# Optimization experiments

Hardware: AMD Instinct MI355X
Metric: run time of the kernel (lower is better)

## Reference

```python
import jax, jax.numpy as jnp
import numpy as np

E = 512        # embedding_dim
HEADS = 8
PD = 32        # patch_dim
STRIDE = 16    # unfold stride (hard-coded in source)
P = 16         # max regions per image (padded)
NCLS = 3       # num_classes
LN_EPS = 1e-5


def layer_norm(x, g, b):
    mu = x.mean(-1, keepdims=True)
    v = ((x - mu) ** 2).mean(-1, keepdims=True)
    return (x - mu) / jnp.sqrt(v + LN_EPS) * g + b


def patch2vec(x, Wr, br):
    # x: [N, C, PD, PD]; AdaptiveAvgPool3d to (C//4, PD//2, PD//2) with exact
    # integer ratios == block-mean pooling, then Linear(fvector, E).
    N, C, H, W = x.shape
    y = x.reshape(N, C // 4, 4, H // 2, 2, W // 2, 2).mean(axis=(2, 4, 6))
    return y.reshape(N, -1) @ Wr.T + br


def mha(q_in, kv_in, Wqkv, bqkv, Wo, bo):
    # torch nn.MultiheadAttention, batch_first=True
    B, Pq, _ = q_in.shape
    L = kv_in.shape[1]
    hd = E // HEADS
    Wq, Wk, Wv = Wqkv[:E], Wqkv[E:2 * E], Wqkv[2 * E:]
    bq, bk, bv = bqkv[:E], bqkv[E:2 * E], bqkv[2 * E:]
    q = (q_in @ Wq.T + bq).reshape(B, Pq, HEADS, hd)
    k = (kv_in @ Wk.T + bk).reshape(B, L, HEADS, hd)
    v = (kv_in @ Wv.T + bv).reshape(B, L, HEADS, hd)
    scores = jnp.einsum('bphd,blhd->bhpl', q, k) / jnp.sqrt(jnp.asarray(hd, q.dtype))
    attn = jax.nn.softmax(scores, axis=-1)
    out = jnp.einsum('bhpl,blhd->bphd', attn, v).reshape(B, Pq, E)
    return out @ Wo.T + bo


def setup_inputs() -> dict:
    key = jax.random.key(0)
    ks = jax.random.split(key, 12)
    B, C, H, W = 8, 64, 256, 256
    fv = (C // 4) * (PD // 2) * (PD // 2)  # 4096
    s = lambda n: 1.0 / np.sqrt(n)
    return {
        'features': jax.random.normal(ks[0], (B, C, H, W), jnp.float32),
        'probs': jax.random.uniform(ks[1], (B, NCLS, H, W), jnp.float32),
        'patches': jax.random.normal(ks[2], (B, P, C, PD, PD), jnp.float32),
        'masks': jax.random.randint(ks[3], (B, H, W), 0, P + 1, jnp.int32),
        'ln_g': jnp.ones((E,), jnp.float32),
        'ln_b': jnp.zeros((E,), jnp.float32),
        'Wr': jax.random.normal(ks[4], (E, fv), jnp.float32) * s(fv),
        'br': jnp.zeros((E,), jnp.float32),
        'Wqkv': jax.random.normal(ks[5], (3 * E, E), jnp.float32) * s(E),
        'bqkv': jnp.zeros((3 * E,), jnp.float32),
        'Wo': jax.random.normal(ks[6], (E, E), jnp.float32) * s(E),
        'bo': jnp.zeros((E,), jnp.float32),
        'Wm': jax.random.normal(ks[7], (E, E), jnp.float32) * s(E),
        'bm': jnp.zeros((E,), jnp.float32),
        'Wc': jax.random.normal(ks[8], (NCLS - 1, E), jnp.float32) * s(E),
        'bc': jnp.zeros((NCLS - 1,), jnp.float32),
    }


def reference(features, probs, patches, masks, ln_g, ln_b, Wr, br,
              Wqkv, bqkv, Wo, bo, Wm, bm, Wc, bc):
    B, C, H, W = features.shape
    # ---- unfold features into overlapping PDxPD blocks, stride 16 ----
    n = (H - PD) // STRIDE + 1  # 15
    rows = (jnp.arange(n) * STRIDE)[:, None] + jnp.arange(PD)[None, :]  # [n, PD]
    xb = features[:, :, rows, :]          # [B, C, n, PD, W]
    blocks = xb[:, :, :, :, rows]         # [B, C, n, PD, n, PD]
    blocks = blocks.transpose(0, 2, 4, 1, 3, 5).reshape(B, n * n, C, PD, PD)
    L = n * n

    # ---- shared Patch2vec embedding + shared LayerNorm ----
    pe = layer_norm(patch2vec(patches.reshape(B * P, C, PD, PD), Wr, br).reshape(B, P, E), ln_g, ln_b)
    be = layer_norm(patch2vec(blocks.reshape(B * L, C, PD, PD), Wr, br).reshape(B, L, E), ln_g, ln_b)

    # ---- attention + residual MLP ----
    attn = mha(pe, be, Wqkv, bqkv, Wo, bo)
    res = layer_norm(attn + pe, ln_g, ln_b)
    x = jax.nn.gelu(res @ Wm.T + bm, approximate=False) + res
    outs = x @ Wc.T + bc  # [B, P, 2]

    # ---- vectorized masked reclassify (regions are disjoint) ----
    labels = masks  # [B, H, W], 0 = background, 1..P = regions
    seg = (labels.astype(jnp.int32) + jnp.arange(B, dtype=jnp.int32)[:, None, None] * (P + 1)).reshape(-1)
    pr = probs.transpose(0, 2, 3, 1).reshape(-1, NCLS)
    sums = jax.ops.segment_sum(pr, seg, num_segments=B * (P + 1)).reshape(B, P + 1, NCLS)
    cnt = jax.ops.segment_sum(jnp.ones((pr.shape[0],), pr.dtype), seg, num_segments=B * (P + 1)).reshape(B, P + 1)
    mean = sums / jnp.maximum(cnt, 1.0)[..., None] + 1e-6  # orig_mean_logits per region
    ml = mean[:, 1:, :]  # [B, P, NCLS], region labels 1..P <-> logits 0..P-1
    new0 = ml[..., 0] / (0.5 * (ml[..., 1] + ml[..., 2])) * outs.mean(-1)
    newv = jnp.stack([new0, outs[..., 0], outs[..., 1]], axis=-1)  # [B, P, 3]
    newv_full = jnp.concatenate([jnp.zeros((B, 1, NCLS), newv.dtype), newv], axis=1)
    vals = newv_full[jnp.arange(B)[:, None], labels.reshape(B, -1)]  # [B, H*W, 3]
    vals = vals.reshape(B, H, W, NCLS).transpose(0, 3, 1, 2)
    return jnp.where((labels > 0)[:, None, :, :], vals, probs)
```

## Files before the change

kernel.cpp:

```cpp
#include <hip/hip_runtime.h>
#include <stdint.h>


typedef __attribute__((ext_vector_type(8))) short bf16x8;
typedef __attribute__((ext_vector_type(4))) float f32x4;

__device__ __forceinline__ unsigned short f2bf(float x) {
    union { float f; unsigned u; } v; v.f = x;
    unsigned r = v.u + 0x7FFFu + ((v.u >> 16) & 1u);
    return (unsigned short)(r >> 16);
}
__device__ __forceinline__ float bf2f(unsigned short x) {
    union { unsigned u; float f; } v; v.u = ((unsigned)x) << 16; return v.f;
}

__device__ __forceinline__ void g2l16(const unsigned short* g, unsigned short* l) {
    __builtin_amdgcn_global_load_lds(
        (const __attribute__((address_space(1))) unsigned int*)g,
        (__attribute__((address_space(3))) unsigned int*)l, 16, 0, 0);
}

__global__ __launch_bounds__(256) void k_pool_features(
    const float* __restrict__ f, unsigned short* __restrict__ gp)
{
    unsigned t = blockIdx.x * 256u + threadIdx.x;
    unsigned q = t & 127u, r = (t >> 7) & 127u, g = (t >> 14) & 15u, b = t >> 18;
    const float2* f2 = (const float2*)f;
    float s = 0.f;
    unsigned cb = b * 64u + g * 4u;
#pragma unroll
    for (int j = 0; j < 4; ++j) {
#pragma unroll
        for (int a = 0; a < 2; ++a) {
            unsigned idx = ((cb + j) * 256u + 2u * r + a) * 256u + 2u * q;
            float2 v = f2[idx >> 1];
            s += v.x + v.y;
        }
    }
    gp[t] = f2bf(s * 0.0625f);
}

__global__ __launch_bounds__(256) void k_pool_patches(
    const float* __restrict__ p, unsigned short* __restrict__ Xb)
{
    unsigned t = blockIdx.x * 256u + threadIdx.x;
    unsigned i = t & 4095u, row = t >> 12;
    unsigned q = i & 15u, r = (i >> 4) & 15u, g = i >> 8;
    const float2* p2 = (const float2*)p;
    float s = 0.f;
    unsigned cb = row * 64u + g * 4u;
#pragma unroll
    for (int j = 0; j < 4; ++j) {
#pragma unroll
        for (int a = 0; a < 2; ++a) {
            unsigned idx = ((cb + j) * 32u + 2u * r + a) * 32u + 2u * q;
            float2 v = p2[idx >> 1];
            s += v.x + v.y;
        }
    }
    Xb[(size_t)row * 4096 + i] = f2bf(s * 0.0625f);
}

__global__ __launch_bounds__(256) void k_gather_blocks(
    const unsigned short* __restrict__ Gp, unsigned short* __restrict__ Xb)
{
    unsigned t = blockIdx.x * 256u + threadIdx.x;
    unsigned grp = t & 511u, row_rel = t >> 9;
    unsigned k0 = grp * 8u;
    unsigned g = k0 >> 8, r = (k0 >> 4) & 15u, q0 = k0 & 15u;
    unsigned b = row_rel / 225u;
    unsigned ij = row_rel - b * 225u;
    unsigned i = ij / 15u, j = ij - i * 15u;
    size_t src = ((size_t)(b * 16u + g) * 128u + i * 8u + r) * 128u + j * 8u + q0;
    size_t dst = (size_t)(128u + row_rel) * 4096u + k0;
    *(uint4*)(Xb + dst) = *(const uint4*)(Gp + src);
}

__global__ __launch_bounds__(256) void k_f2bf_all(
    const float* __restrict__ Wr, const float* __restrict__ Wqkv,
    const float* __restrict__ Wo, const float* __restrict__ Wm,
    unsigned short* __restrict__ oWr, unsigned short* __restrict__ oWqkv,
    unsigned short* __restrict__ oWo, unsigned short* __restrict__ oWm)
{
    int t = blockIdx.x * 256 + threadIdx.x;
    const float* src; unsigned short* dst; int i;
    if (t < 524288)      { src = Wr;   dst = oWr;   i = t; }
    else if (t < 720896) { src = Wqkv; dst = oWqkv; i = t - 524288; }
    else if (t < 786432) { src = Wo;   dst = oWo;   i = t - 720896; }
    else                 { src = Wm;   dst = oWm;   i = t - 786432; }
    float4 v = ((const float4*)src)[i];
    ushort4 o;
    o.x = f2bf(v.x); o.y = f2bf(v.y); o.z = f2bf(v.z); o.w = f2bf(v.w);
    ((ushort4*)dst)[i] = o;
}

__global__ __launch_bounds__(256) void k_gemm128(
    const unsigned short* __restrict__ A, const unsigned short* __restrict__ Bw,
    const float* __restrict__ bias, float* __restrict__ C,
    int M, int N, int K, int klen)
{
    __shared__ __align__(16) unsigned short As[128 * 32];
    __shared__ __align__(16) unsigned short Bs[128 * 32];
    const int tid = threadIdx.x, w = tid >> 6, lane = tid & 63;
    const int nt = blockIdx.x, mt = blockIdx.y, ks = blockIdx.z;
    const int kbase = ks * klen;
    const int l15 = lane & 15, kq = (lane >> 4) * 8;
    const int wm = (w >> 1) * 64, wn = (w & 1) * 64;
    const int srow0 = w * 32, lrow = lane >> 2, lcol = (lane & 3) * 8;

    f32x4 acc[4][4];
#pragma unroll
    for (int i = 0; i < 4; ++i)
#pragma unroll
        for (int j = 0; j < 4; ++j) acc[i][j] = (f32x4){0.f, 0.f, 0.f, 0.f};

    int arow0 = mt * 128, brow0 = nt * 128;
    for (int k0 = 0; k0 < klen; k0 += 32) {
        int kk = kbase + k0;
#pragma unroll
        for (int c = 0; c < 2; ++c) {
            int r = srow0 + c * 16 + lrow;
            int ga = arow0 + r; if (ga > M - 1) ga = M - 1;
            g2l16(A + (size_t)ga * K + kk + lcol, &As[(srow0 + c * 16) * 32]);
            g2l16(Bw + (size_t)(brow0 + r) * K + kk + lcol, &Bs[(srow0 + c * 16) * 32]);
        }
        __syncthreads();
        bf16x8 af[4], bf[4];
#pragma unroll
        for (int i = 0; i < 4; ++i) {
            af[i] = *(const bf16x8*)&As[(wm + 16 * i + l15) * 32 + kq];
            bf[i] = *(const bf16x8*)&Bs[(wn + 16 * i + l15) * 32 + kq];
        }
#pragma unroll
        for (int i = 0; i < 4; ++i)
#pragma unroll
            for (int j = 0; j < 4; ++j)
                acc[i][j] = __builtin_amdgcn_mfma_f32_16x16x32_bf16(af[i], bf[j], acc[i][j], 0, 0, 0);
        __syncthreads();
    }
    float* Cp = C + (size_t)ks * M * N;
#pragma unroll
    for (int i = 0; i < 4; ++i) {
        int rowb = mt * 128 + wm + i * 16 + (lane >> 4) * 4;
#pragma unroll
        for (int j = 0; j < 4; ++j) {
            int col = nt * 128 + wn + j * 16 + l15;
            float bv = bias ? bias[col] : 0.f;
#pragma unroll
            for (int r = 0; r < 4; ++r) {
                int row = rowb + r;
                if (row < M) Cp[(size_t)row * N + col] = acc[i][j][r] + bv;
            }
        }
    }
}

__global__ __launch_bounds__(256) void k_gemm_nt(
    const unsigned short* __restrict__ A, const unsigned short* __restrict__ Bw,
    const float* __restrict__ bias, float* __restrict__ C,
    int M, int N, int K)
{
    __shared__ __align__(16) unsigned short As[64 * 32];
    __shared__ __align__(16) unsigned short Bs[64 * 32];
    const int tid = threadIdx.x;
    const int bm = blockIdx.y, bn = blockIdx.x;
    const int wave = tid >> 6, lane = tid & 63;
    const int wm = (wave >> 1) * 32, wn = (wave & 1) * 32;
    const int l15 = lane & 15, kq = (lane >> 4) * 8;
    const int srow = tid >> 2, scol = (tid & 3) * 8;
    const unsigned short* Ap = A + (size_t)(bm * 64 + srow) * K + scol;
    const unsigned short* Bp = Bw + (size_t)(bn * 64 + srow) * K + scol;

    f32x4 acc[2][2];
#pragma unroll
    for (int i = 0; i < 2; ++i)
#pragma unroll
        for (int j = 0; j < 2; ++j) acc[i][j] = (f32x4){0.f, 0.f, 0.f, 0.f};

    for (int k0 = 0; k0 < K; k0 += 32) {
        *(uint4*)&As[srow * 32 + scol] = *(const uint4*)(Ap + k0);
        *(uint4*)&Bs[srow * 32 + scol] = *(const uint4*)(Bp + k0);
        __syncthreads();
        bf16x8 a0 = *(const bf16x8*)&As[(wm + l15) * 32 + kq];
        bf16x8 a1 = *(const bf16x8*)&As[(wm + 16 + l15) * 32 + kq];
        bf16x8 b0 = *(const bf16x8*)&Bs[(wn + l15) * 32 + kq];
        bf16x8 b1 = *(const bf16x8*)&Bs[(wn + 16 + l15) * 32 + kq];
        acc[0][0] = __builtin_amdgcn_mfma_f32_16x16x32_bf16(a0, b0, acc[0][0], 0, 0, 0);
        acc[0][1] = __builtin_amdgcn_mfma_f32_16x16x32_bf16(a0, b1, acc[0][1], 0, 0, 0);
        acc[1][0] = __builtin_amdgcn_mfma_f32_16x16x32_bf16(a1, b0, acc[1][0], 0, 0, 0);
        acc[1][1] = __builtin_amdgcn_mfma_f32_16x16x32_bf16(a1, b1, acc[1][1], 0, 0, 0);
        __syncthreads();
    }
#pragma unroll
    for (int it = 0; it < 2; ++it) {
        int rowb = bm * 64 + wm + it * 16 + (lane >> 4) * 4;
#pragma unroll
        for (int iu = 0; iu < 2; ++iu) {
            int col = bn * 64 + wn + iu * 16 + l15;
            float bv = bias[col];
#pragma unroll
            for (int r = 0; r < 4; ++r) {
                int row = rowb + r;
                if (row < M) C[(size_t)row * N + col] = acc[it][iu][r] + bv;
            }
        }
    }
}

__global__ __launch_bounds__(256) void k_lnred(
    const float* __restrict__ Yp, const float* __restrict__ br,
    const float* __restrict__ gg, const float* __restrict__ bb,
    float* __restrict__ outF, unsigned short* __restrict__ outB, int rows)
{
    int wave = threadIdx.x >> 6, lane = threadIdx.x & 63;
    int row = blockIdx.x * 4 + wave;
    if (row >= rows) return;
    size_t base = (size_t)row * 512 + lane * 8;
    float v[8];
    { const float* bp = br + lane * 8;
      float4 a = *(const float4*)bp, b = *(const float4*)(bp + 4);
      v[0]=a.x; v[1]=a.y; v[2]=a.z; v[3]=a.w; v[4]=b.x; v[5]=b.y; v[6]=b.z; v[7]=b.w; }
#pragma unroll
    for (int s = 0; s < 4; ++s) {
        const float* xp = Yp + (size_t)s * rows * 512 + base;
        float4 a = *(const float4*)xp, b = *(const float4*)(xp + 4);
        v[0]+=a.x; v[1]+=a.y; v[2]+=a.z; v[3]+=a.w; v[4]+=b.x; v[5]+=b.y; v[6]+=b.z; v[7]+=b.w;
    }
    float s = 0.f;
#pragma unroll
    for (int i = 0; i < 8; ++i) s += v[i];
#pragma unroll
    for (int m = 32; m; m >>= 1) s += __shfl_xor(s, m, 64);
    float mu = s * (1.f / 512.f);
    float sq = 0.f;
#pragma unroll
    for (int i = 0; i < 8; ++i) { float d = v[i] - mu; sq += d * d; }
#pragma unroll
    for (int m = 32; m; m >>= 1) sq += __shfl_xor(sq, m, 64);
    float rstd = rsqrtf(sq * (1.f / 512.f) + 1e-5f);
    const float* gp = gg + lane * 8;
    const float* bp2 = bb + lane * 8;
    float4 g0 = *(const float4*)gp, g1 = *(const float4*)(gp + 4);
    float4 b0 = *(const float4*)bp2, b1 = *(const float4*)(bp2 + 4);
    float ga[8] = {g0.x,g0.y,g0.z,g0.w,g1.x,g1.y,g1.z,g1.w};
    float ba[8] = {b0.x,b0.y,b0.z,b0.w,b1.x,b1.y,b1.z,b1.w};
    float o[8];
#pragma unroll
    for (int i = 0; i < 8; ++i) o[i] = (v[i] - mu) * rstd * ga[i] + ba[i];
    float* ofp = outF + base;
    float4 w0; w0.x=o[0]; w0.y=o[1]; w0.z=o[2]; w0.w=o[3];
    float4 w1; w1.x=o[4]; w1.y=o[5]; w1.z=o[6]; w1.w=o[7];
    *(float4*)ofp = w0; *(float4*)(ofp + 4) = w1;
    unsigned short* obp = outB + base;
    ushort4 u0, u1;
    u0.x=f2bf(o[0]); u0.y=f2bf(o[1]); u0.z=f2bf(o[2]); u0.w=f2bf(o[3]);
    u1.x=f2bf(o[4]); u1.y=f2bf(o[5]); u1.z=f2bf(o[6]); u1.w=f2bf(o[7]);
    ((ushort4*)obp)[0] = u0; ((ushort4*)obp)[1] = u1;
}

__global__ __launch_bounds__(256) void k_ln(
    const float* __restrict__ X, const float* __restrict__ R,
    const float* __restrict__ gg, const float* __restrict__ bb,
    float* __restrict__ outF, unsigned short* __restrict__ outB, int rows)
{
    int wave = threadIdx.x >> 6, lane = threadIdx.x & 63;
    int row = blockIdx.x * 4 + wave;
    if (row >= rows) return;
    size_t base = (size_t)row * 512 + lane * 8;
    const float* xp = X + base;
    float v[8];
    { float4 a = *(const float4*)xp, b = *(const float4*)(xp + 4);
      v[0]=a.x; v[1]=a.y; v[2]=a.z; v[3]=a.w; v[4]=b.x; v[5]=b.y; v[6]=b.z; v[7]=b.w; }
    { const float* rp = R + base;
      float4 a = *(const float4*)rp, b = *(const float4*)(rp + 4);
      v[0]+=a.x; v[1]+=a.y; v[2]+=a.z; v[3]+=a.w; v[4]+=b.x; v[5]+=b.y; v[6]+=b.z; v[7]+=b.w; }
    float s = 0.f;
#pragma unroll
    for (int i = 0; i < 8; ++i) s += v[i];
#pragma unroll
    for (int m = 32; m; m >>= 1) s += __shfl_xor(s, m, 64);
    float mu = s * (1.f / 512.f);
    float sq = 0.f;
#pragma unroll
    for (int i = 0; i < 8; ++i) { float d = v[i] - mu; sq += d * d; }
#pragma unroll
    for (int m = 32; m; m >>= 1) sq += __shfl_xor(sq, m, 64);
    float rstd = rsqrtf(sq * (1.f / 512.f) + 1e-5f);
    const float* gp = gg + lane * 8;
    const float* bp = bb + lane * 8;
    float4 g0 = *(const float4*)gp, g1 = *(const float4*)(gp + 4);
    float4 b0 = *(const float4*)bp, b1 = *(const float4*)(bp + 4);
    float ga[8] = {g0.x,g0.y,g0.z,g0.w,g1.x,g1.y,g1.z,g1.w};
    float ba[8] = {b0.x,b0.y,b0.z,b0.w,b1.x,b1.y,b1.z,b1.w};
    float o[8];
#pragma unroll
    for (int i = 0; i < 8; ++i) o[i] = (v[i] - mu) * rstd * ga[i] + ba[i];
    float* ofp = outF + base;
    float4 w0; w0.x=o[0]; w0.y=o[1]; w0.z=o[2]; w0.w=o[3];
    float4 w1; w1.x=o[4]; w1.y=o[5]; w1.z=o[6]; w1.w=o[7];
    *(float4*)ofp = w0; *(float4*)(ofp + 4) = w1;
    unsigned short* obp = outB + base;
    ushort4 u0, u1;
    u0.x=f2bf(o[0]); u0.y=f2bf(o[1]); u0.z=f2bf(o[2]); u0.w=f2bf(o[3]);
    u1.x=f2bf(o[4]); u1.y=f2bf(o[5]); u1.z=f2bf(o[6]); u1.w=f2bf(o[7]);
    ((ushort4*)obp)[0] = u0; ((ushort4*)obp)[1] = u1;
}

__global__ __launch_bounds__(256) void k_attn(
    const float* __restrict__ QKV, unsigned short* __restrict__ attn_bf)
{
    int b = blockIdx.x, h = blockIdx.y;
    __shared__ __align__(16) float qs[16 * 64];
    __shared__ unsigned short Vs[225 * 64];
    __shared__ float sc[16 * 225];
    int t = threadIdx.x;
    for (int i = t; i < 1024; i += 256) {
        int p = i >> 6, d = i & 63;
        qs[i] = QKV[(size_t)(b * 16 + p) * 1536 + h * 64 + d];
    }
    for (int i = t; i < 14400; i += 256) {
        int l = i >> 6, d = i & 63;
        Vs[i] = f2bf(QKV[(size_t)(128 + b * 225 + l) * 1536 + 1024 + h * 64 + d]);
    }
    __syncthreads();
    for (int i = t; i < 3600; i += 256) {
        int p = i / 225, l = i - p * 225;
        const float4* k4 = (const float4*)(QKV + (size_t)(128 + b * 225 + l) * 1536 + 512 + h * 64);
        const float4* q4 = (const float4*)&qs[p * 64];
        float s = 0.f;
#pragma unroll
        for (int d = 0; d < 16; ++d) {
            float4 kk = k4[d], qq = q4[d];
            s += kk.x * qq.x + kk.y * qq.y + kk.z * qq.z + kk.w * qq.w;
        }
        sc[p * 225 + l] = s * 0.125f;
    }
    __syncthreads();
    int lane = t & 63, wave = t >> 6;
    int p = wave * 4 + (lane >> 4), sub = lane & 15;
    float m = -1e30f;
    for (int l = sub; l < 225; l += 16) m = fmaxf(m, sc[p * 225 + l]);
#pragma unroll
    for (int off = 8; off; off >>= 1) m = fmaxf(m, __shfl_xor(m, off, 16));
    float s = 0.f;
    for (int l = sub; l < 225; l += 16) {
        float e = __expf(sc[p * 225 + l] - m);
        sc[p * 225 + l] = e; s += e;
    }
#pragma unroll
    for (int off = 8; off; off >>= 1) s += __shfl_xor(s, off, 16);
    float inv = 1.f / s;
    for (int l = sub; l < 225; l += 16) sc[p * 225 + l] *= inv;
    __syncthreads();
    for (int i = t; i < 1024; i += 256) {
        int p2 = i >> 6, d = i & 63;
        float o = 0.f;
        for (int l = 0; l < 225; ++l) o += sc[p2 * 225 + l] * bf2f(Vs[l * 64 + d]);
        attn_bf[(size_t)(b * 16 + p2) * 512 + h * 64 + d] = f2bf(o);
    }
}

__global__ __launch_bounds__(256) void k_wc(
    const float* __restrict__ m1, const float* __restrict__ res,
    const float* __restrict__ Wc, const float* __restrict__ bc,
    float* __restrict__ outs)
{
    int wave = threadIdx.x >> 6, lane = threadIdx.x & 63;
    int row = blockIdx.x * 4 + wave;
    size_t base = (size_t)row * 512 + lane * 8;
    const float* mp = m1 + base;
    const float* rp = res + base;
    const float* w0p = Wc + lane * 8;
    const float* w1p = Wc + 512 + lane * 8;
    float4 ma = *(const float4*)mp, mb = *(const float4*)(mp + 4);
    float4 ra = *(const float4*)rp, rb = *(const float4*)(rp + 4);
    float4 wa0 = *(const float4*)w0p, wb0 = *(const float4*)(w0p + 4);
    float4 wa1 = *(const float4*)w1p, wb1 = *(const float4*)(w1p + 4);
    float mv[8] = {ma.x,ma.y,ma.z,ma.w,mb.x,mb.y,mb.z,mb.w};
    float rv[8] = {ra.x,ra.y,ra.z,ra.w,rb.x,rb.y,rb.z,rb.w};
    float w0[8] = {wa0.x,wa0.y,wa0.z,wa0.w,wb0.x,wb0.y,wb0.z,wb0.w};
    float w1[8] = {wa1.x,wa1.y,wa1.z,wa1.w,wb1.x,wb1.y,wb1.z,wb1.w};
    float s0 = 0.f, s1 = 0.f;
#pragma unroll
    for (int i = 0; i < 8; ++i) {
        float v = mv[i];
        float x = 0.5f * v * (1.f + erff(v * 0.70710678118654752f)) + rv[i];
        s0 += x * w0[i]; s1 += x * w1[i];
    }
#pragma unroll
    for (int m = 32; m; m >>= 1) {
        s0 += __shfl_xor(s0, m, 64);
        s1 += __shfl_xor(s1, m, 64);
    }
    if (lane == 0) {
        outs[row * 2 + 0] = s0 + bc[0];
        outs[row * 2 + 1] = s1 + bc[1];
    }
}

__global__ void k_zero(float* __restrict__ p, int n) {
    int t = blockIdx.x * blockDim.x + threadIdx.x;
    if (t < n) p[t] = 0.f;
}

__global__ __launch_bounds__(256) void k_hist(
    const int* __restrict__ masks, const float* __restrict__ probs,
    float* __restrict__ sums, float* __restrict__ cnt)
{
    __shared__ float ls[68];
    int t = threadIdx.x;
    if (t < 68) ls[t] = 0.f;
    __syncthreads();
    int b = blockIdx.x >> 6, chunk = blockIdx.x & 63;
    int base = chunk * 1024;
    for (int it = 0; it < 4; ++it) {
        int px = base + it * 256 + t;
        int lab = masks[b * 65536 + px];
        atomicAdd(&ls[lab * 3 + 0], probs[(size_t)(b * 3 + 0) * 65536 + px]);
        atomicAdd(&ls[lab * 3 + 1], probs[(size_t)(b * 3 + 1) * 65536 + px]);
        atomicAdd(&ls[lab * 3 + 2], probs[(size_t)(b * 3 + 2) * 65536 + px]);
        atomicAdd(&ls[51 + lab], 1.f);
    }
    __syncthreads();
    if (t < 51)       atomicAdd(&sums[b * 51 + t], ls[t]);
    else if (t < 68)  atomicAdd(&cnt[b * 17 + t - 51], ls[t]);
}

__global__ void k_newv(
    const float* __restrict__ seg, const float* __restrict__ outs,
    float* __restrict__ newv)
{
    int t = threadIdx.x;
    if (t >= 136) return;
    int lab = t % 17;
    const float* sums = seg;
    const float* cnt  = seg + 408;
    if (lab == 0) { newv[t*3+0] = 0.f; newv[t*3+1] = 0.f; newv[t*3+2] = 0.f; return; }
    int b = t / 17;
    float c  = fmaxf(cnt[t], 1.f);
    float m0 = sums[t*3+0] / c + 1e-6f;
    float m1 = sums[t*3+1] / c + 1e-6f;
    float m2 = sums[t*3+2] / c + 1e-6f;
    int p = lab - 1;
    float o0 = outs[(b*16+p)*2+0], o1 = outs[(b*16+p)*2+1];
    float new0 = m0 / (0.5f * (m1 + m2)) * (0.5f * (o0 + o1));
    newv[t*3+0] = new0; newv[t*3+1] = o0; newv[t*3+2] = o1;
}

__global__ __launch_bounds__(256) void k_out(
    const int* __restrict__ masks, const float* __restrict__ probs,
    const float* __restrict__ newv, float* __restrict__ out)
{
    int t = blockIdx.x * 256 + threadIdx.x;
    int b = t >> 16, hw = t & 65535;
    int lab = masks[t];
    if (lab > 0) {
        const float* nv = newv + (size_t)(b * 17 + lab) * 3;
        out[(size_t)(b*3+0)*65536 + hw] = nv[0];
        out[(size_t)(b*3+1)*65536 + hw] = nv[1];
        out[(size_t)(b*3+2)*65536 + hw] = nv[2];
    } else {
        out[(size_t)(b*3+0)*65536 + hw] = probs[(size_t)(b*3+0)*65536 + hw];
        out[(size_t)(b*3+1)*65536 + hw] = probs[(size_t)(b*3+1)*65536 + hw];
        out[(size_t)(b*3+2)*65536 + hw] = probs[(size_t)(b*3+2)*65536 + hw];
    }
}

extern "C" void kernel_launch(void* const* d_in, const int* in_sizes, int n_in,
                              void* d_out, int out_size, void* d_ws, size_t ws_size,
                              hipStream_t stream)
{
    const float* features = (const float*)d_in[0];
    const float* probs    = (const float*)d_in[1];
    const float* patches  = (const float*)d_in[2];
    const int*   masks    = (const int*)d_in[3];
    const float* ln_g     = (const float*)d_in[4];
    const float* ln_b     = (const float*)d_in[5];
    const float* Wr       = (const float*)d_in[6];
    const float* br       = (const float*)d_in[7];
    const float* Wqkv     = (const float*)d_in[8];
    const float* bqkv     = (const float*)d_in[9];
    const float* Wo       = (const float*)d_in[10];
    const float* bo       = (const float*)d_in[11];
    const float* Wm       = (const float*)d_in[12];
    const float* bm       = (const float*)d_in[13];
    const float* Wc       = (const float*)d_in[14];
    const float* bc       = (const float*)d_in[15];
    float* out = (float*)d_out;

    char* w = (char*)d_ws;
    size_t off = 0;
    auto alloc = [&](size_t bytes) -> char* {
        char* p = w + off;
        off += (bytes + 255) & ~(size_t)255;
        return p;
    };
    unsigned short* Gp     = (unsigned short*)alloc((size_t)2097152 * 2);
    unsigned short* Xb     = (unsigned short*)alloc((size_t)1928 * 4096 * 2);
    unsigned short* Wr_b   = (unsigned short*)alloc((size_t)2097152 * 2);
    unsigned short* Wqkv_b = (unsigned short*)alloc((size_t)786432 * 2);
    unsigned short* Wo_b   = (unsigned short*)alloc((size_t)262144 * 2);
    unsigned short* Wm_b   = (unsigned short*)alloc((size_t)262144 * 2);
    float* Yp   = (float*)alloc((size_t)4 * 1928 * 512 * 4);
    float* LNf  = (float*)alloc((size_t)1928 * 512 * 4);
    unsigned short* LNb = (unsigned short*)alloc((size_t)1928 * 512 * 2);
    float* QKV  = (float*)alloc((size_t)1928 * 1536 * 4);
    unsigned short* attnb = (unsigned short*)alloc((size_t)65536 * 2);
    float* Zo   = (float*)alloc((size_t)65536 * 4);
    float* resf = (float*)alloc((size_t)65536 * 4);
    unsigned short* resb = (unsigned short*)alloc((size_t)65536 * 2);
    float* M1   = (float*)alloc((size_t)65536 * 4);
    float* outsB = (float*)alloc((size_t)256 * 4);
    float* seg   = (float*)alloc((size_t)544 * 4);
    float* newv  = (float*)alloc((size_t)408 * 4);

    k_zero<<<3, 256, 0, stream>>>(seg, 544);

    k_pool_features<<<8192, 256, 0, stream>>>(features, Gp);
    k_pool_patches<<<2048, 256, 0, stream>>>(patches, Xb);
    k_gather_blocks<<<3600, 256, 0, stream>>>(Gp, Xb);
    k_f2bf_all<<<3328, 256, 0, stream>>>(Wr, Wqkv, Wo, Wm, Wr_b, Wqkv_b, Wo_b, Wm_b);

    k_gemm128<<<dim3(4, 16, 4), 256, 0, stream>>>(Xb, Wr_b, nullptr, Yp, 1928, 512, 4096, 1024);
    k_lnred<<<482, 256, 0, stream>>>(Yp, br, ln_g, ln_b, LNf, LNb, 1928);

    k_gemm128<<<dim3(12, 16, 1), 256, 0, stream>>>(LNb, Wqkv_b, bqkv, QKV, 1928, 1536, 512, 512);

    k_attn<<<dim3(8, 8), 256, 0, stream>>>(QKV, attnb);

    k_gemm_nt<<<dim3(8, 2), 256, 0, stream>>>(attnb, Wo_b, bo, Zo, 128, 512, 512);
    k_ln<<<32, 256, 0, stream>>>(Zo, LNf, ln_g, ln_b, resf, resb, 128);

    k_gemm_nt<<<dim3(8, 2), 256, 0, stream>>>(resb, Wm_b, bm, M1, 128, 512, 512);
    k_wc<<<32, 256, 0, stream>>>(M1, resf, Wc, bc, outsB);

    k_hist<<<512, 256, 0, stream>>>(masks, probs, seg, seg + 408);
    k_newv<<<1, 256, 0, stream>>>(seg, outsB, newv);
    k_out<<<2048, 256, 0, stream>>>(masks, probs, newv, out);
}
```

Baseline: 406.5 us.

## Fuse prep kernels, deepen split-K, split attention by query group, fold newv into output

Pool, patch-pool, weight-conversion and seg-zeroing kernels are merged into one launch, and k_newv is folded into k_out through shared memory, which cuts the launch count. The Wr GEMM split-K goes from 4 to 8 and the QKV GEMM gains a 2-way split-K. The two QKV partials and the bias are summed inside the attention kernel. Attention now runs over 4 query groups per (batch, head), stages K as bf16 in LDS, and uses one wave per query row for softmax. k_hist uses per-wave LDS bins to reduce atomic contention, at the cost of extra partial-sum traffic and lower K precision.

```diff
diff --git a/kernel.cpp b/kernel.cpp
--- a/kernel.cpp
+++ b/kernel.cpp
@@ -20,45 +20,60 @@
         (__attribute__((address_space(3))) unsigned int*)l, 16, 0, 0);
 }
 
-__global__ __launch_bounds__(256) void k_pool_features(
-    const float* __restrict__ f, unsigned short* __restrict__ gp)
-{
-    unsigned t = blockIdx.x * 256u + threadIdx.x;
-    unsigned q = t & 127u, r = (t >> 7) & 127u, g = (t >> 14) & 15u, b = t >> 18;
-    const float2* f2 = (const float2*)f;
-    float s = 0.f;
-    unsigned cb = b * 64u + g * 4u;
-#pragma unroll
-    for (int j = 0; j < 4; ++j) {
-#pragma unroll
-        for (int a = 0; a < 2; ++a) {
-            unsigned idx = ((cb + j) * 256u + 2u * r + a) * 256u + 2u * q;
-            float2 v = f2[idx >> 1];
-            s += v.x + v.y;
-        }
-    }
-    gp[t] = f2bf(s * 0.0625f);
-}
-
-__global__ __launch_bounds__(256) void k_pool_patches(
-    const float* __restrict__ p, unsigned short* __restrict__ Xb)
-{
-    unsigned t = blockIdx.x * 256u + threadIdx.x;
-    unsigned i = t & 4095u, row = t >> 12;
-    unsigned q = i & 15u, r = (i >> 4) & 15u, g = i >> 8;
-    const float2* p2 = (const float2*)p;
-    float s = 0.f;
-    unsigned cb = row * 64u + g * 4u;
-#pragma unroll
-    for (int j = 0; j < 4; ++j) {
-#pragma unroll
-        for (int a = 0; a < 2; ++a) {
-            unsigned idx = ((cb + j) * 32u + 2u * r + a) * 32u + 2u * q;
-            float2 v = p2[idx >> 1];
-            s += v.x + v.y;
-        }
-    }
-    Xb[(size_t)row * 4096 + i] = f2bf(s * 0.0625f);
+__global__ __launch_bounds__(256) void k_prep(
+    const float* __restrict__ f, const float* __restrict__ p,
+    const float* __restrict__ Wr, const float* __restrict__ Wqkv,
+    const float* __restrict__ Wo, const float* __restrict__ Wm,
+    unsigned short* __restrict__ gp, unsigned short* __restrict__ Xb,
+    unsigned short* __restrict__ oWr, unsigned short* __restrict__ oWqkv,
+    unsigned short* __restrict__ oWo, unsigned short* __restrict__ oWm,
+    float* __restrict__ seg)
+{
+    int blk = blockIdx.x, tid = threadIdx.x;
+    if (blk < 8192) {
+        if (blk == 0) for (int i = tid; i < 544; i += 256) seg[i] = 0.f;
+        unsigned t = blk * 256u + tid;
+        unsigned q = t & 127u, r = (t >> 7) & 127u, g = (t >> 14) & 15u, b = t >> 18;
+        const float2* f2 = (const float2*)f;
+        float s = 0.f;
+        unsigned cb = b * 64u + g * 4u;
+#pragma unroll
+        for (int j = 0; j < 4; ++j)
+#pragma unroll
+            for (int a = 0; a < 2; ++a) {
+                unsigned idx = ((cb + j) * 256u + 2u * r + a) * 256u + 2u * q;
+                float2 v = f2[idx >> 1];
+                s += v.x + v.y;
+            }
+        gp[t] = f2bf(s * 0.0625f);
+    } else if (blk < 10240) {
+        unsigned t = (blk - 8192) * 256u + tid;
+        unsigned i = t & 4095u, row = t >> 12;
+        unsigned q = i & 15u, r = (i >> 4) & 15u, g = i >> 8;
+        const float2* p2 = (const float2*)p;
+        float s = 0.f;
+        unsigned cb = row * 64u + g * 4u;
+#pragma unroll
+        for (int j = 0; j < 4; ++j)
+#pragma unroll
+            for (int a = 0; a < 2; ++a) {
+                unsigned idx = ((cb + j) * 32u + 2u * r + a) * 32u + 2u * q;
+                float2 v = p2[idx >> 1];
+                s += v.x + v.y;
+            }
+        Xb[(size_t)row * 4096 + i] = f2bf(s * 0.0625f);
+    } else {
+        int t = (blk - 10240) * 256 + tid;
+        const float* src; unsigned short* dst; int i;
+        if (t < 524288)      { src = Wr;   dst = oWr;   i = t; }
+        else if (t < 720896) { src = Wqkv; dst = oWqkv; i = t - 524288; }
+        else if (t < 786432) { src = Wo;   dst = oWo;   i = t - 720896; }
+        else                 { src = Wm;   dst = oWm;   i = t - 786432; }
+        float4 v = ((const float4*)src)[i];
+        ushort4 o;
+        o.x = f2bf(v.x); o.y = f2bf(v.y); o.z = f2bf(v.z); o.w = f2bf(v.w);
+        ((ushort4*)dst)[i] = o;
+    }
 }
 
 __global__ __launch_bounds__(256) void k_gather_blocks(
@@ -74,24 +89,6 @@
     size_t src = ((size_t)(b * 16u + g) * 128u + i * 8u + r) * 128u + j * 8u + q0;
     size_t dst = (size_t)(128u + row_rel) * 4096u + k0;
     *(uint4*)(Xb + dst) = *(const uint4*)(Gp + src);
-}
-
-__global__ __launch_bounds__(256) void k_f2bf_all(
-    const float* __restrict__ Wr, const float* __restrict__ Wqkv,
-    const float* __restrict__ Wo, const float* __restrict__ Wm,
-    unsigned short* __restrict__ oWr, unsigned short* __restrict__ oWqkv,
-    unsigned short* __restrict__ oWo, unsigned short* __restrict__ oWm)
-{
-    int t = blockIdx.x * 256 + threadIdx.x;
-    const float* src; unsigned short* dst; int i;
-    if (t < 524288)      { src = Wr;   dst = oWr;   i = t; }
-    else if (t < 720896) { src = Wqkv; dst = oWqkv; i = t - 524288; }
-    else if (t < 786432) { src = Wo;   dst = oWo;   i = t - 720896; }
-    else                 { src = Wm;   dst = oWm;   i = t - 786432; }
-    float4 v = ((const float4*)src)[i];
-    ushort4 o;
-    o.x = f2bf(v.x); o.y = f2bf(v.y); o.z = f2bf(v.z); o.w = f2bf(v.w);
-    ((ushort4*)dst)[i] = o;
 }
 
 __global__ __launch_bounds__(256) void k_gemm128(
@@ -210,7 +207,8 @@
 __global__ __launch_bounds__(256) void k_lnred(
     const float* __restrict__ Yp, const float* __restrict__ br,
     const float* __restrict__ gg, const float* __restrict__ bb,
-    float* __restrict__ outF, unsigned short* __restrict__ outB, int rows)
+    float* __restrict__ outF, unsigned short* __restrict__ outB,
+    int rows, int nsplit)
 {
     int wave = threadIdx.x >> 6, lane = threadIdx.x & 63;
     int row = blockIdx.x * 4 + wave;
@@ -220,8 +218,7 @@
     { const float* bp = br + lane * 8;
       float4 a = *(const float4*)bp, b = *(const float4*)(bp + 4);
       v[0]=a.x; v[1]=a.y; v[2]=a.z; v[3]=a.w; v[4]=b.x; v[5]=b.y; v[6]=b.z; v[7]=b.w; }
-#pragma unroll
-    for (int s = 0; s < 4; ++s) {
+    for (int s = 0; s < nsplit; ++s) {
         const float* xp = Yp + (size_t)s * rows * 512 + base;
         float4 a = *(const float4*)xp, b = *(const float4*)(xp + 4);
         v[0]+=a.x; v[1]+=a.y; v[2]+=a.z; v[3]+=a.w; v[4]+=b.x; v[5]+=b.y; v[6]+=b.z; v[7]+=b.w;
@@ -307,56 +304,65 @@
 }
 
 __global__ __launch_bounds__(256) void k_attn(
-    const float* __restrict__ QKV, unsigned short* __restrict__ attn_bf)
-{
-    int b = blockIdx.x, h = blockIdx.y;
-    __shared__ __align__(16) float qs[16 * 64];
-    __shared__ unsigned short Vs[225 * 64];
-    __shared__ float sc[16 * 225];
-    int t = threadIdx.x;
-    for (int i = t; i < 1024; i += 256) {
-        int p = i >> 6, d = i & 63;
-        qs[i] = QKV[(size_t)(b * 16 + p) * 1536 + h * 64 + d];
-    }
+    const float* __restrict__ QKVp, const float* __restrict__ bqkv,
+    unsigned short* __restrict__ attn_bf)
+{
+    const int b = blockIdx.x, h = blockIdx.y, pz = blockIdx.z;
+    const size_t PS = (size_t)1928 * 1536;
+    __shared__ __align__(16) float qs[4 * 64];
+    __shared__ __align__(16) unsigned short Ks[225 * 68];
+    __shared__ __align__(16) unsigned short Vs[225 * 64];
+    __shared__ float sc[4 * 225];
+    const int t = threadIdx.x;
+
+    {
+        int p = t >> 6, d = t & 63;
+        size_t idx = (size_t)(b * 16 + pz * 4 + p) * 1536 + h * 64 + d;
+        qs[t] = QKVp[idx] + QKVp[PS + idx] + bqkv[h * 64 + d];
+    }
+    float bk = bqkv[512 + h * 64 + (t & 63)];
+    float bv = bqkv[1024 + h * 64 + (t & 63)];
     for (int i = t; i < 14400; i += 256) {
         int l = i >> 6, d = i & 63;
-        Vs[i] = f2bf(QKV[(size_t)(128 + b * 225 + l) * 1536 + 1024 + h * 64 + d]);
+        size_t base = (size_t)(128 + b * 225 + l) * 1536 + h * 64 + d;
+        Ks[l * 68 + d] = f2bf(QKVp[base + 512] + QKVp[PS + base + 512] + bk);
+        Vs[l * 64 + d] = f2bf(QKVp[base + 1024] + QKVp[PS + base + 1024] + bv);
     }
     __syncthreads();
-    for (int i = t; i < 3600; i += 256) {
+    for (int i = t; i < 900; i += 256) {
         int p = i / 225, l = i - p * 225;
-        const float4* k4 = (const float4*)(QKV + (size_t)(128 + b * 225 + l) * 1536 + 512 + h * 64);
+        const ushort4* k4 = (const ushort4*)&Ks[l * 68];
         const float4* q4 = (const float4*)&qs[p * 64];
         float s = 0.f;
 #pragma unroll
         for (int d = 0; d < 16; ++d) {
-            float4 kk = k4[d], qq = q4[d];
-            s += kk.x * qq.x + kk.y * qq.y + kk.z * qq.z + kk.w * qq.w;
+            ushort4 kk = k4[d]; float4 qq = q4[d];
+            s += bf2f(kk.x) * qq.x + bf2f(kk.y) * qq.y
+               + bf2f(kk.z) * qq.z + bf2f(kk.w) * qq.w;
         }
         sc[p * 225 + l] = s * 0.125f;
     }
     __syncthreads();
-    int lane = t & 63, wave = t >> 6;
-    int p = wave * 4 + (lane >> 4), sub = lane & 15;
-    float m = -1e30f;
-    for (int l = sub; l < 225; l += 16) m = fmaxf(m, sc[p * 225 + l]);
-#pragma unroll
-    for (int off = 8; off; off >>= 1) m = fmaxf(m, __shfl_xor(m, off, 16));
-    float s = 0.f;
-    for (int l = sub; l < 225; l += 16) {
-        float e = __expf(sc[p * 225 + l] - m);
-        sc[p * 225 + l] = e; s += e;
-    }
-#pragma unroll
-    for (int off = 8; off; off >>= 1) s += __shfl_xor(s, off, 16);
-    float inv = 1.f / s;
-    for (int l = sub; l < 225; l += 16) sc[p * 225 + l] *= inv;
+    const int lane = t & 63, wave = t >> 6;
+    {
+        float* row = &sc[wave * 225];
+        float m = -1e30f;
+        for (int l = lane; l < 225; l += 64) m = fmaxf(m, row[l]);
+#pragma unroll
+        for (int off = 32; off; off >>= 1) m = fmaxf(m, __shfl_xor(m, off, 64));
+        float s = 0.f;
+        for (int l = lane; l < 225; l += 64) { float e = __expf(row[l] - m); row[l] = e; s += e; }
+#pragma unroll
+        for (int off = 32; off; off >>= 1) s += __shfl_xor(s, off, 64);
+        float inv = 1.f / s;
+        for (int l = lane; l < 225; l += 64) row[l] *= inv;
+    }
     __syncthreads();
-    for (int i = t; i < 1024; i += 256) {
-        int p2 = i >> 6, d = i & 63;
+    {
         float o = 0.f;
-        for (int l = 0; l < 225; ++l) o += sc[p2 * 225 + l] * bf2f(Vs[l * 64 + d]);
-        attn_bf[(size_t)(b * 16 + p2) * 512 + h * 64 + d] = f2bf(o);
+        const float* scp = &sc[wave * 225];
+        for (int l = 0; l < 225; ++l) o += scp[l] * bf2f(Vs[l * 64 + lane]);
+        attn_bf[(size_t)(b * 16 + pz * 4 + wave) * 512 + h * 64 + lane] = f2bf(o);
     }
 }
 
@@ -398,71 +404,67 @@
     }
 }
 
-__global__ void k_zero(float* __restrict__ p, int n) {
-    int t = blockIdx.x * blockDim.x + threadIdx.x;
-    if (t < n) p[t] = 0.f;
-}
-
 __global__ __launch_bounds__(256) void k_hist(
     const int* __restrict__ masks, const float* __restrict__ probs,
     float* __restrict__ sums, float* __restrict__ cnt)
 {
-    __shared__ float ls[68];
-    int t = threadIdx.x;
-    if (t < 68) ls[t] = 0.f;
+    __shared__ float ls[4][68];
+    int t = threadIdx.x, wave = t >> 6;
+    for (int i = t; i < 272; i += 256) ((float*)ls)[i] = 0.f;
     __syncthreads();
     int b = blockIdx.x >> 6, chunk = blockIdx.x & 63;
     int base = chunk * 1024;
     for (int it = 0; it < 4; ++it) {
         int px = base + it * 256 + t;
         int lab = masks[b * 65536 + px];
-        atomicAdd(&ls[lab * 3 + 0], probs[(size_t)(b * 3 + 0) * 65536 + px]);
-        atomicAdd(&ls[lab * 3 + 1], probs[(size_t)(b * 3 + 1) * 65536 + px]);
-        atomicAdd(&ls[lab * 3 + 2], probs[(size_t)(b * 3 + 2) * 65536 + px]);
-        atomicAdd(&ls[51 + lab], 1.f);
+        atomicAdd(&ls[wave][lab * 3 + 0], probs[(size_t)(b * 3 + 0) * 65536 + px]);
+        atomicAdd(&ls[wave][lab * 3 + 1], probs[(size_t)(b * 3 + 1) * 65536 + px]);
+        atomicAdd(&ls[wave][lab * 3 + 2], probs[(size_t)(b * 3 + 2) * 65536 + px]);
+        atomicAdd(&ls[wave][51 + lab], 1.f);
     }
     __syncthreads();
-    if (t < 51)       atomicAdd(&sums[b * 51 + t], ls[t]);
-    else if (t < 68)  atomicAdd(&cnt[b * 17 + t - 51], ls[t]);
-}
-
-__global__ void k_newv(
-    const float* __restrict__ seg, const float* __restrict__ outs,
-    float* __restrict__ newv)
-{
-    int t = threadIdx.x;
-    if (t >= 136) return;
-    int lab = t % 17;
-    const float* sums = seg;
-    const float* cnt  = seg + 408;
-    if (lab == 0) { newv[t*3+0] = 0.f; newv[t*3+1] = 0.f; newv[t*3+2] = 0.f; return; }
-    int b = t / 17;
-    float c  = fmaxf(cnt[t], 1.f);
-    float m0 = sums[t*3+0] / c + 1e-6f;
-    float m1 = sums[t*3+1] / c + 1e-6f;
-    float m2 = sums[t*3+2] / c + 1e-6f;
-    int p = lab - 1;
-    float o0 = outs[(b*16+p)*2+0], o1 = outs[(b*16+p)*2+1];
-    float new0 = m0 / (0.5f * (m1 + m2)) * (0.5f * (o0 + o1));
-    newv[t*3+0] = new0; newv[t*3+1] = o0; newv[t*3+2] = o1;
+    if (t < 68) {
+        float v = ls[0][t] + ls[1][t] + ls[2][t] + ls[3][t];
+        if (t < 51) atomicAdd(&sums[b * 51 + t], v);
+        else        atomicAdd(&cnt[b * 17 + t - 51], v);
+    }
 }
 
 __global__ __launch_bounds__(256) void k_out(
     const int* __restrict__ masks, const float* __restrict__ probs,
-    const float* __restrict__ newv, float* __restrict__ out)
-{
-    int t = blockIdx.x * 256 + threadIdx.x;
-    int b = t >> 16, hw = t & 65535;
-    int lab = masks[t];
+    const float* __restrict__ seg, const float* __restrict__ outs,
+    float* __restrict__ out)
+{
+    __shared__ float nv[17 * 3];
+    int tid = threadIdx.x;
+    int b = blockIdx.x >> 8;
+    if (tid < 17) {
+        int lab = tid;
+        if (lab == 0) { nv[0] = 0.f; nv[1] = 0.f; nv[2] = 0.f; }
+        else {
+            float c  = fmaxf(seg[408 + b * 17 + lab], 1.f);
+            float m0 = seg[(b * 17 + lab) * 3 + 0] / c + 1e-6f;
+            float m1 = seg[(b * 17 + lab) * 3 + 1] / c + 1e-6f;
+            float m2 = seg[(b * 17 + lab) * 3 + 2] / c + 1e-6f;
+            int p = lab - 1;
+            float o0 = outs[(b * 16 + p) * 2 + 0], o1 = outs[(b * 16 + p) * 2 + 1];
+            nv[lab * 3 + 0] = m0 / (0.5f * (m1 + m2)) * (0.5f * (o0 + o1));
+            nv[lab * 3 + 1] = o0;
+            nv[lab * 3 + 2] = o1;
+        }
+    }
+    __syncthreads();
+    int px = (blockIdx.x & 255) * 256 + tid;
+    int gl = b * 65536 + px;
+    int lab = masks[gl];
     if (lab > 0) {
-        const float* nv = newv + (size_t)(b * 17 + lab) * 3;
-        out[(size_t)(b*3+0)*65536 + hw] = nv[0];
-        out[(size_t)(b*3+1)*65536 + hw] = nv[1];
-        out[(size_t)(b*3+2)*65536 + hw] = nv[2];
+        out[(size_t)(b*3+0)*65536 + px] = nv[lab*3+0];
+        out[(size_t)(b*3+1)*65536 + px] = nv[lab*3+1];
+        out[(size_t)(b*3+2)*65536 + px] = nv[lab*3+2];
     } else {
-        out[(size_t)(b*3+0)*65536 + hw] = probs[(size_t)(b*3+0)*65536 + hw];
-        out[(size_t)(b*3+1)*65536 + hw] = probs[(size_t)(b*3+1)*65536 + hw];
-        out[(size_t)(b*3+2)*65536 + hw] = probs[(size_t)(b*3+2)*65536 + hw];
+        out[(size_t)(b*3+0)*65536 + px] = probs[(size_t)(b*3+0)*65536 + px];
+        out[(size_t)(b*3+1)*65536 + px] = probs[(size_t)(b*3+1)*65536 + px];
+        out[(size_t)(b*3+2)*65536 + px] = probs[(size_t)(b*3+2)*65536 + px];
     }
 }
 
@@ -501,10 +503,10 @@
     unsigned short* Wqkv_b = (unsigned short*)alloc((size_t)786432 * 2);
     unsigned short* Wo_b   = (unsigned short*)alloc((size_t)262144 * 2);
     unsigned short* Wm_b   = (unsigned short*)alloc((size_t)262144 * 2);
-    float* Yp   = (float*)alloc((size_t)4 * 1928 * 512 * 4);
+    float* Yp   = (float*)alloc((size_t)8 * 1928 * 512 * 4);
     float* LNf  = (float*)alloc((size_t)1928 * 512 * 4);
     unsigned short* LNb = (unsigned short*)alloc((size_t)1928 * 512 * 2);
-    float* QKV  = (float*)alloc((size_t)1928 * 1536 * 4);
+    float* QKV  = (float*)alloc((size_t)2 * 1928 * 1536 * 4);
     unsigned short* attnb = (unsigned short*)alloc((size_t)65536 * 2);
     float* Zo   = (float*)alloc((size_t)65536 * 4);
     float* resf = (float*)alloc((size_t)65536 * 4);
@@ -512,29 +514,18 @@
     float* M1   = (float*)alloc((size_t)65536 * 4);
     float* outsB = (float*)alloc((size_t)256 * 4);
     float* seg   = (float*)alloc((size_t)544 * 4);
-    float* newv  = (float*)alloc((size_t)408 * 4);
-
-    k_zero<<<3, 256, 0, stream>>>(seg, 544);
-
-    k_pool_features<<<8192, 256, 0, stream>>>(features, Gp);
-    k_pool_patches<<<2048, 256, 0, stream>>>(patches, Xb);
+
+    k_prep<<<13568, 256, 0, stream>>>(features, patches, Wr, Wqkv, Wo, Wm,
+                                      Gp, Xb, Wr_b, Wqkv_b, Wo_b, Wm_b, seg);
     k_gather_blocks<<<3600, 256, 0, stream>>>(Gp, Xb);
-    k_f2bf_all<<<3328, 256, 0, stream>>>(Wr, Wqkv, Wo, Wm, Wr_b, Wqkv_b, Wo_b, Wm_b);
-
-    k_gemm128<<<dim3(4, 16, 4), 256, 0, stream>>>(Xb, Wr_b, nullptr, Yp, 1928, 512, 4096, 1024);
-    k_lnred<<<482, 256, 0, stream>>>(Yp, br, ln_g, ln_b, LNf, LNb, 1928);
-
-    k_gemm128<<<dim3(12, 16, 1), 256, 0, stream>>>(LNb, Wqkv_b, bqkv, QKV, 1928, 1536, 512, 512);
-
-    k_attn<<<dim3(8, 8), 256, 0, stream>>>(QKV, attnb);
-
+    k_gemm128<<<dim3(4, 16, 8), 256, 0, stream>>>(Xb, Wr_b, nullptr, Yp, 1928, 512, 4096, 512);
+    k_lnred<<<482, 256, 0, stream>>>(Yp, br, ln_g, ln_b, LNf, LNb, 1928, 8);
+    k_gemm128<<<dim3(12, 16, 2), 256, 0, stream>>>(LNb, Wqkv_b, nullptr, QKV, 1928, 1536, 512, 256);
+    k_attn<<<dim3(8, 8, 4), 256, 0, stream>>>(QKV, bqkv, attnb);
     k_gemm_nt<<<dim3(8, 2), 256, 0, stream>>>(attnb, Wo_b, bo, Zo, 128, 512, 512);
     k_ln<<<32, 256, 0, stream>>>(Zo, LNf, ln_g, ln_b, resf, resb, 128);
-
     k_gemm_nt<<<dim3(8, 2), 256, 0, stream>>>(resb, Wm_b, bm, M1, 128, 512, 512);
     k_wc<<<32, 256, 0, stream>>>(M1, resf, Wc, bc, outsB);
-
     k_hist<<<512, 256, 0, stream>>>(masks, probs, seg, seg + 408);
-    k_newv<<<1, 256, 0, stream>>>(seg, outsB, newv);
-    k_out<<<2048, 256, 0, stream>>>(masks, probs, newv, out);
-}
+    k_out<<<2048, 256, 0, stream>>>(masks, probs, seg, outsB, out);
+}
```

Result: faster. 368.0 us (-9.5%).
